# Performance work log

Hardware: AMD Instinct MI355X
Metric: run time of the kernel (lower is better)

## Reference

```python
import jax, jax.numpy as jnp
import numpy as np

N = 50000
IN_CH = 256
HEADS = 8
OUT_CH = 32
E = 800000


def setup_inputs() -> dict:
    key = jax.random.key(0)
    k1, k2, k3, k4, k5 = jax.random.split(key, 5)
    x = jax.random.normal(k1, (N, IN_CH), dtype=jnp.float32)
    edge_index = jax.random.randint(k2, (2, E), 0, N, dtype=jnp.int64)
    # torch Linear(in, heads*out, bias=False): weight [heads*out, in]
    W = jax.random.normal(k3, (HEADS * OUT_CH, IN_CH), dtype=jnp.float32) / np.sqrt(IN_CH)
    # xavier_uniform over (1, heads, out)
    bound = float(np.sqrt(6.0 / (HEADS + OUT_CH)))
    attn_l = jax.random.uniform(k4, (1, HEADS, OUT_CH), minval=-bound, maxval=bound, dtype=jnp.float32)
    attn_r = jax.random.uniform(k5, (1, HEADS, OUT_CH), minval=-bound, maxval=bound, dtype=jnp.float32)
    return {"x": x, "edge_index": edge_index, "W": W, "attn_l": attn_l, "attn_r": attn_r}


def reference(x, edge_index, W, attn_l, attn_r):
    num_nodes = x.shape[0]
    # node-level projection: [N, H, C]
    xp = (x @ W.T).reshape(num_nodes, HEADS, OUT_CH).astype(jnp.float32)
    # add self loops
    loops = jnp.arange(num_nodes, dtype=edge_index.dtype)
    src = jnp.concatenate([edge_index[0], loops])
    dst = jnp.concatenate([edge_index[1], loops])
    # edge attention logits per head: [Etot, H]
    alpha_l = (xp * attn_l).sum(-1)[src]
    alpha_r = (xp * attn_r).sum(-1)[dst]
    alpha = jax.nn.leaky_relu(alpha_l + alpha_r, negative_slope=0.2)
    # global per-head max subtraction (as in the original), then scatter softmax over dst
    alpha = jnp.exp(alpha - alpha.max(axis=0, keepdims=True))
    alpha_sum = jax.ops.segment_sum(alpha, dst, num_segments=num_nodes)  # [N, H]
    alpha = alpha / jnp.maximum(alpha_sum[dst], 1e-6)
    # weighted aggregation: scatter-add alpha * x_src to dst, all heads at once
    msgs = alpha[:, :, None] * xp[src]  # [Etot, H, C]
    out = jax.ops.segment_sum(msgs, dst, num_segments=num_nodes)  # [N, H, C]
    return out.reshape(num_nodes, HEADS * OUT_CH)
```

## Files before the change

### kernel.cpp

```cpp
#include <hip/hip_runtime.h>
#include <math.h>

#define IN_CH   256
#define HEADS   8
#define OUT_CH  32
#define CAP     64

typedef __attribute__((ext_vector_type(8))) short s16x8;
typedef __attribute__((ext_vector_type(4))) float f32x4;

__device__ inline short f2bf(float f) {
  unsigned u = __builtin_bit_cast(unsigned, f);
  u += 0x7fffu + ((u >> 16) & 1u);
  return (short)(u >> 16);
}
__device__ inline float bf2f(unsigned short u) {
  unsigned v = ((unsigned)u) << 16;
  return __builtin_bit_cast(float, v);
}

__global__ __launch_bounds__(256) void prep(
    const float* __restrict__ W, short* __restrict__ Wb,
    int* __restrict__ cnt) {
  const int b = blockIdx.x;
  if (b < 64) {
    const int i = (b * 256 + (int)threadIdx.x) * 4;
    float4 v = *(const float4*)(W + i);
    ushort4 o;
    o.x = (unsigned short)f2bf(v.x);
    o.y = (unsigned short)f2bf(v.y);
    o.z = (unsigned short)f2bf(v.z);
    o.w = (unsigned short)f2bf(v.w);
    *(ushort4*)(Wb + i) = o;
  } else {
    const int i = ((b - 64) * 256 + (int)threadIdx.x) * 4;
    *(int4*)(cnt + i) = make_int4(0, 0, 0, 0);
  }
}

__global__ __launch_bounds__(256) void fill_buckets(
    const int* __restrict__ src_idx, const int* __restrict__ dst_idx,
    int* __restrict__ cnt, int* __restrict__ csrs, int E, int n) {
  const int e = blockIdx.x * 256 + (int)threadIdx.x;
  if (e >= E + n) return;
  int s, d;
  if (e < E) {
    s = src_idx[e];
    d = dst_idx[e];
  } else {
    s = d = e - E;
  }
  const int p = atomicAdd(&cnt[d], 1);
  if (p < CAP) csrs[d * CAP + p] = s;
}

__global__ __launch_bounds__(256) void gemm(
    const float* __restrict__ x, const short* __restrict__ Wb,
    const float* __restrict__ attn_l, const float* __restrict__ attn_r,
    short* __restrict__ xpb, float* __restrict__ al, float* __restrict__ ar,
    int n) {
  __shared__ short Ws[8 * 256 * 8];
  __shared__ short Xs[8 * 64 * 8];
  const int tid  = threadIdx.x;
  const int wave = tid >> 6;
  const int lane = tid & 63;
  const int nrow = lane & 15;
  const int kq   = lane >> 4;
  const int node0 = blockIdx.x * 64;

  f32x4 acc[4][4];
#pragma unroll
  for (int i = 0; i < 4; ++i)
#pragma unroll
    for (int j = 0; j < 4; ++j) acc[i][j] = (f32x4){0.f, 0.f, 0.f, 0.f};

  for (int k0 = 0; k0 < IN_CH; k0 += 64) {
    __syncthreads();
#pragma unroll
    for (int s = 0; s < 8; ++s) {
      s16x8 v = *(const s16x8*)(Wb + (size_t)tid * IN_CH + k0 + s * 8);
      *(s16x8*)&Ws[(s * 256 + tid) * 8] = v;
    }
#pragma unroll
    for (int p = 0; p < 2; ++p) {
      const int c = p * 256 + tid;
      const int row = c >> 3, o = c & 7;
      int grow = node0 + row;
      if (grow >= n) grow = n - 1;
      const float* xr = x + (size_t)grow * IN_CH + k0 + o * 8;
      float4 lo = *(const float4*)xr;
      float4 hi = *(const float4*)(xr + 4);
      s16x8 v;
      v[0] = f2bf(lo.x); v[1] = f2bf(lo.y); v[2] = f2bf(lo.z); v[3] = f2bf(lo.w);
      v[4] = f2bf(hi.x); v[5] = f2bf(hi.y); v[6] = f2bf(hi.z); v[7] = f2bf(hi.w);
      *(s16x8*)&Xs[(o * 64 + row) * 8] = v;
    }
    __syncthreads();
#pragma unroll
    for (int kk = 0; kk < 2; ++kk) {
      const int o = kk * 4 + kq;
      s16x8 af[4], bf[4];
#pragma unroll
      for (int i = 0; i < 4; ++i)
        af[i] = *(const s16x8*)&Ws[(o * 256 + wave * 64 + i * 16 + nrow) * 8];
#pragma unroll
      for (int j = 0; j < 4; ++j)
        bf[j] = *(const s16x8*)&Xs[(o * 64 + j * 16 + nrow) * 8];
#pragma unroll
      for (int i = 0; i < 4; ++i)
#pragma unroll
        for (int j = 0; j < 4; ++j)
          acc[i][j] = __builtin_amdgcn_mfma_f32_16x16x32_bf16(
              af[i], bf[j], acc[i][j], 0, 0, 0);
    }
  }

  float pl[4][2] = {}, pr[4][2] = {};
#pragma unroll
  for (int i = 0; i < 4; ++i) {
    const int oc = wave * 64 + i * 16 + kq * 4;
    const float4 la = *(const float4*)(attn_l + oc);
    const float4 ra = *(const float4*)(attn_r + oc);
    const int hh = i >> 1;
#pragma unroll
    for (int j = 0; j < 4; ++j) {
      const int node = node0 + j * 16 + nrow;
      ushort4 st;
      st.x = (unsigned short)f2bf(acc[i][j][0]);
      st.y = (unsigned short)f2bf(acc[i][j][1]);
      st.z = (unsigned short)f2bf(acc[i][j][2]);
      st.w = (unsigned short)f2bf(acc[i][j][3]);
      if (node < n) *(ushort4*)(xpb + (size_t)node * IN_CH + oc) = st;
      pl[j][hh] += acc[i][j][0] * la.x + acc[i][j][1] * la.y +
                   acc[i][j][2] * la.z + acc[i][j][3] * la.w;
      pr[j][hh] += acc[i][j][0] * ra.x + acc[i][j][1] * ra.y +
                   acc[i][j][2] * ra.z + acc[i][j][3] * ra.w;
    }
  }
#pragma unroll
  for (int j = 0; j < 4; ++j)
#pragma unroll
    for (int hh = 0; hh < 2; ++hh) {
      float vl = pl[j][hh], vr = pr[j][hh];
      vl += __shfl_xor(vl, 16); vl += __shfl_xor(vl, 32);
      vr += __shfl_xor(vr, 16); vr += __shfl_xor(vr, 32);
      const int node = node0 + j * 16 + nrow;
      if (kq == 0 && node < n) {
        al[node * HEADS + wave * 2 + hh] = vl;
        ar[node * HEADS + wave * 2 + hh] = vr;
      }
    }
}

__global__ __launch_bounds__(256) void gat_gather(
    const int* __restrict__ csrs, const int* __restrict__ cntp,
    const short* __restrict__ xpb, const float* __restrict__ al,
    const float* __restrict__ ar, float* __restrict__ out, int n) {
  const int gid = blockIdx.x * blockDim.x + threadIdx.x;
  const int d = gid >> 6;
  if (d >= n) return;
  const int lane = gid & 63;
  const int half = lane >> 5;
  const int cl = lane & 31;
  const int h = cl >> 2;
  const int start = d * CAP;
  int cnt = cntp[d];
  if (cnt > CAP) cnt = CAP;
  const float ard = ar[d * HEADS + h];

  float acc[8] = {0.f, 0.f, 0.f, 0.f, 0.f, 0.f, 0.f, 0.f};
  float denom = 0.f;
  for (int jb = 0; jb < cnt; jb += 4) {
    const int j0 = jb + half;
    const int j1 = jb + 2 + half;
    const bool v0 = j0 < cnt, v1 = j1 < cnt;
    const int s0 = v0 ? csrs[start + j0] : d;
    const int s1 = v1 ? csrs[start + j1] : d;
    const s16x8 u0 = *(const s16x8*)(xpb + (size_t)s0 * IN_CH + cl * 8);
    const s16x8 u1 = *(const s16x8*)(xpb + (size_t)s1 * IN_CH + cl * 8);
    float a0 = al[s0 * HEADS + h] + ard;
    float a1 = al[s1 * HEADS + h] + ard;
    a0 = a0 > 0.f ? a0 : 0.2f * a0;
    a1 = a1 > 0.f ? a1 : 0.2f * a1;
    const float w0 = v0 ? __expf(a0) : 0.f;
    const float w1 = v1 ? __expf(a1) : 0.f;
    denom += w0 + w1;
#pragma unroll
    for (int k = 0; k < 8; ++k) {
      acc[k] = fmaf(w0, bf2f((unsigned short)u0[k]), acc[k]);
      acc[k] = fmaf(w1, bf2f((unsigned short)u1[k]), acc[k]);
    }
  }
  denom += __shfl_xor(denom, 32);
#pragma unroll
  for (int k = 0; k < 8; ++k) acc[k] += __shfl_xor(acc[k], 32);
  if (half == 0) {
    const float inv = 1.f / fmaxf(denom, 1e-6f);
    f32x4 v0 = {acc[0] * inv, acc[1] * inv, acc[2] * inv, acc[3] * inv};
    f32x4 v1 = {acc[4] * inv, acc[5] * inv, acc[6] * inv, acc[7] * inv};
    float* op = out + (size_t)d * IN_CH + cl * 8;
    __builtin_nontemporal_store(v0, (f32x4*)op);
    __builtin_nontemporal_store(v1, (f32x4*)(op + 4));
  }
}

extern "C" void kernel_launch(void* const* d_in, const int* in_sizes, int n_in,
                              void* d_out, int out_size, void* d_ws,
                              size_t ws_size, hipStream_t stream) {
  const float* x      = (const float*)d_in[0];
  const int*   ei     = (const int*)d_in[1];
  const float* W      = (const float*)d_in[2];
  const float* attn_l = (const float*)d_in[3];
  const float* attn_r = (const float*)d_in[4];
  float* out = (float*)d_out;

  const int n = in_sizes[0] / IN_CH;
  const int E = in_sizes[1] / 2;
  const int Etot = E + n;

  short* xpb  = (short*)d_ws;
  short* Wb   = xpb + (size_t)n * IN_CH;
  float* al   = (float*)(Wb + IN_CH * IN_CH);
  float* ar   = al + (size_t)n * HEADS;
  int*   cnt  = (int*)(ar + (size_t)n * HEADS);
  int*   csrs = cnt + n;

  prep<<<113, 256, 0, stream>>>(W, Wb, cnt);

  fill_buckets<<<(Etot + 255) / 256, 256, 0, stream>>>(
      ei, ei + E, cnt, csrs, E, n);

  const int gemm_blocks = (n + 63) / 64;
  gemm<<<gemm_blocks, 256, 0, stream>>>(x, Wb, attn_l, attn_r, xpb, al, ar, n);

  const long long g_threads = (long long)n * 64;
  gat_gather<<<(int)((g_threads + 255) / 256), 256, 0, stream>>>(
      csrs, cnt, xpb, al, ar, out, n);
}
```

Before: 250.2 us.

## Fuse edge bucketing into GEMM kernel and widen gather batching

```diff
diff --git a/kernel.cpp b/kernel.cpp
--- a/kernel.cpp
+++ b/kernel.cpp
@@ -13,10 +13,6 @@
   unsigned u = __builtin_bit_cast(unsigned, f);
   u += 0x7fffu + ((u >> 16) & 1u);
   return (short)(u >> 16);
-}
-__device__ inline float bf2f(unsigned short u) {
-  unsigned v = ((unsigned)u) << 16;
-  return __builtin_bit_cast(float, v);
 }
 
 __global__ __launch_bounds__(256) void prep(
@@ -38,30 +34,32 @@
   }
 }
 
-__global__ __launch_bounds__(256) void fill_buckets(
-    const int* __restrict__ src_idx, const int* __restrict__ dst_idx,
-    int* __restrict__ cnt, int* __restrict__ csrs, int E, int n) {
-  const int e = blockIdx.x * 256 + (int)threadIdx.x;
-  if (e >= E + n) return;
-  int s, d;
-  if (e < E) {
-    s = src_idx[e];
-    d = dst_idx[e];
-  } else {
-    s = d = e - E;
-  }
-  const int p = atomicAdd(&cnt[d], 1);
-  if (p < CAP) csrs[d * CAP + p] = s;
-}
-
-__global__ __launch_bounds__(256) void gemm(
+__global__ __launch_bounds__(256) void gemm_fill(
     const float* __restrict__ x, const short* __restrict__ Wb,
     const float* __restrict__ attn_l, const float* __restrict__ attn_r,
     short* __restrict__ xpb, float* __restrict__ al, float* __restrict__ ar,
-    int n) {
+    const int* __restrict__ src_idx, const int* __restrict__ dst_idx,
+    int* __restrict__ cnt, int* __restrict__ csrs, int E, int n) {
+  const int tid = threadIdx.x;
+
+  {
+    const int Etot = E + n;
+    const int stride = (int)gridDim.x * 256;
+    for (int e = (int)blockIdx.x * 256 + tid; e < Etot; e += stride) {
+      int s, d;
+      if (e < E) {
+        s = src_idx[e];
+        d = dst_idx[e];
+      } else {
+        s = d = e - E;
+      }
+      const int p = atomicAdd(&cnt[d], 1);
+      if (p < CAP) csrs[d * CAP + p] = s;
+    }
+  }
+
   __shared__ short Ws[8 * 256 * 8];
   __shared__ short Xs[8 * 64 * 8];
-  const int tid  = threadIdx.x;
   const int wave = tid >> 6;
   const int lane = tid & 63;
   const int nrow = lane & 15;
@@ -150,6 +148,18 @@
         ar[node * HEADS + wave * 2 + hh] = vr;
       }
     }
+}
+
+__device__ inline void acc8(float w, const s16x8& u, float* acc) {
+  const unsigned* p = (const unsigned*)&u;
+#pragma unroll
+  for (int j = 0; j < 4; ++j) {
+    const unsigned v = p[j];
+    const float flo = __builtin_bit_cast(float, v << 16);
+    const float fhi = __builtin_bit_cast(float, v & 0xFFFF0000u);
+    acc[2 * j]     = fmaf(w, flo, acc[2 * j]);
+    acc[2 * j + 1] = fmaf(w, fhi, acc[2 * j + 1]);
+  }
 }
 
 __global__ __launch_bounds__(256) void gat_gather(
@@ -170,26 +180,27 @@
 
   float acc[8] = {0.f, 0.f, 0.f, 0.f, 0.f, 0.f, 0.f, 0.f};
   float denom = 0.f;
-  for (int jb = 0; jb < cnt; jb += 4) {
-    const int j0 = jb + half;
-    const int j1 = jb + 2 + half;
-    const bool v0 = j0 < cnt, v1 = j1 < cnt;
-    const int s0 = v0 ? csrs[start + j0] : d;
-    const int s1 = v1 ? csrs[start + j1] : d;
-    const s16x8 u0 = *(const s16x8*)(xpb + (size_t)s0 * IN_CH + cl * 8);
-    const s16x8 u1 = *(const s16x8*)(xpb + (size_t)s1 * IN_CH + cl * 8);
-    float a0 = al[s0 * HEADS + h] + ard;
-    float a1 = al[s1 * HEADS + h] + ard;
-    a0 = a0 > 0.f ? a0 : 0.2f * a0;
-    a1 = a1 > 0.f ? a1 : 0.2f * a1;
-    const float w0 = v0 ? __expf(a0) : 0.f;
-    const float w1 = v1 ? __expf(a1) : 0.f;
-    denom += w0 + w1;
-#pragma unroll
-    for (int k = 0; k < 8; ++k) {
-      acc[k] = fmaf(w0, bf2f((unsigned short)u0[k]), acc[k]);
-      acc[k] = fmaf(w1, bf2f((unsigned short)u1[k]), acc[k]);
-    }
+  for (int jb = 0; jb < cnt; jb += 8) {
+    const int base = jb + half * 4;
+    const int4 q = *(const int4*)(csrs + start + base);
+    const int* qp = (const int*)&q;
+    int s[4];
+#pragma unroll
+    for (int i = 0; i < 4; ++i) s[i] = (base + i < cnt) ? qp[i] : d;
+    s16x8 u[4];
+#pragma unroll
+    for (int i = 0; i < 4; ++i)
+      u[i] = *(const s16x8*)(xpb + (size_t)s[i] * IN_CH + cl * 8);
+    float w[4];
+#pragma unroll
+    for (int i = 0; i < 4; ++i) {
+      float a = al[s[i] * HEADS + h] + ard;
+      a = a > 0.f ? a : 0.2f * a;
+      w[i] = (base + i < cnt) ? __expf(a) : 0.f;
+      denom += w[i];
+    }
+#pragma unroll
+    for (int i = 0; i < 4; ++i) acc8(w[i], u[i], acc);
   }
   denom += __shfl_xor(denom, 32);
 #pragma unroll
@@ -216,7 +227,6 @@
 
   const int n = in_sizes[0] / IN_CH;
   const int E = in_sizes[1] / 2;
-  const int Etot = E + n;
 
   short* xpb  = (short*)d_ws;
   short* Wb   = xpb + (size_t)n * IN_CH;
@@ -227,11 +237,9 @@
 
   prep<<<113, 256, 0, stream>>>(W, Wb, cnt);
 
-  fill_buckets<<<(Etot + 255) / 256, 256, 0, stream>>>(
-      ei, ei + E, cnt, csrs, E, n);
-
   const int gemm_blocks = (n + 63) / 64;
-  gemm<<<gemm_blocks, 256, 0, stream>>>(x, Wb, attn_l, attn_r, xpb, al, ar, n);
+  gemm_fill<<<gemm_blocks, 256, 0, stream>>>(
+      x, Wb, attn_l, attn_r, xpb, al, ar, ei, ei + E, cnt, csrs, E, n);
 
   const long long g_threads = (long long)n * 64;
   gat_gather<<<(int)((g_threads + 255) / 256), 256, 0, stream>>>(
```

Measured after the change: 249.5 us. No clear change (-0.3%).
